# Kernel tuning notes

Hardware: AMD Instinct MI355X
Metric: run time of the kernel (lower is better)

Reference implementation:

```python
import jax, jax.numpy as jnp
import numpy as np

N_NODES = 100000
N_EDGES = 1600000
IN_FEATS = 64
HIDDEN = 128


def setup_inputs() -> dict:
    key = jax.random.key(0)
    k1, k2, k3, k4 = jax.random.split(key, 4)
    X = jax.random.normal(k1, (N_NODES, IN_FEATS), dtype=jnp.float32)
    edge_index = jax.random.randint(k2, (2, N_EDGES), 0, N_NODES, dtype=jnp.int64)
    W1 = jax.random.normal(k3, (IN_FEATS, HIDDEN), dtype=jnp.float32) * (1.0 / np.sqrt(IN_FEATS))
    b1 = jnp.zeros((HIDDEN,), dtype=jnp.float32)
    W2 = jax.random.normal(k4, (HIDDEN, 1), dtype=jnp.float32) * (1.0 / np.sqrt(HIDDEN))
    b2 = jnp.zeros((1,), dtype=jnp.float32)
    return {"X": X, "edge_index": edge_index, "W1": W1, "b1": b1, "W2": W2, "b2": b2}


def _gcn_conv(X, src, dst, norm, W, b, n_nodes):
    # GCNConv: out = D^{-1/2} (A + I) D^{-1/2} (X @ W) + b
    h = X @ W                       # [N, out_feats]
    msg = h[src] * norm[:, None]    # gather + per-edge scale
    out = jax.ops.segment_sum(msg, dst, num_segments=n_nodes)
    return out + b


def _norm_and_loops(edge_index, n_nodes):
    # add self loops and compute symmetric normalization coefficients
    loop = jnp.arange(n_nodes, dtype=edge_index.dtype)
    src = jnp.concatenate([edge_index[0], loop])
    dst = jnp.concatenate([edge_index[1], loop])
    deg = jax.ops.segment_sum(jnp.ones_like(dst, dtype=jnp.float32), dst,
                              num_segments=n_nodes)  # deg >= 1 (self loop)
    dinv = jax.lax.rsqrt(deg)
    norm = dinv[src] * dinv[dst]    # [E + N]
    return src, dst, norm


def reference(X, edge_index, W1, b1, W2, b2):
    n_nodes = X.shape[0]
    src, dst, norm = _norm_and_loops(edge_index, n_nodes)
    h = jax.nn.relu(_gcn_conv(X, src, dst, norm, W1, b1, n_nodes))
    # dropout omitted (stochastic; identity for deterministic reference)
    out = _gcn_conv(h, src, dst, norm, W2, b2, n_nodes)
    return out
```

## Files before the change

kernel.cpp:

```cpp
#include <hip/hip_runtime.h>
#include <hip/hip_fp16.h>


#define NNODES 100000
#define INF 64
#define HID 128
#define MAXBK 128
#define TILE_E 16384

using half8 = __attribute__((ext_vector_type(8))) _Float16;
using f32x4 = __attribute__((ext_vector_type(4))) float;

__global__ __launch_bounds__(1024) void k_thist(const int* __restrict__ dstA,
                                                int* __restrict__ tileCnt, int nE,
                                                const float* __restrict__ W1,
                                                _Float16* __restrict__ W1t, int nt) {
    __shared__ int h[MAXBK];
    int tid = threadIdx.x;
    int bx = blockIdx.x;
    if (bx == nt) {
        for (int i = tid; i < HID * INF; i += 1024) {
            int nCol = i >> 6;
            int k = i & 63;
            W1t[i] = (_Float16)W1[k * HID + nCol];
        }
        return;
    }
    if (tid < MAXBK) h[tid] = 0;
    __syncthreads();
    int base = bx * TILE_E;
#pragma unroll
    for (int k = 0; k < 16; ++k) {
        int e = base + k * 1024 + tid;
        if (e < nE) atomicAdd(&h[((unsigned)dstA[e]) >> 10], 1);
    }
    __syncthreads();
    if (tid < MAXBK) tileCnt[bx * MAXBK + tid] = h[tid];
}

__global__ __launch_bounds__(1024) void k_bscan(const int* __restrict__ tileCnt,
                                                int* __restrict__ tileBase,
                                                int* __restrict__ bBase,
                                                int* __restrict__ rowPtr,
                                                int n, int nbk, int nt) {
    __shared__ int part[8][MAXBK];
    __shared__ int colScan[MAXBK];
    int b = threadIdx.x & (MAXBK - 1);
    int tg = threadIdx.x >> 7;
    int cpg = (nt + 7) / 8;
    int tlo = tg * cpg, thi = min(tlo + cpg, nt);
    int sum = 0;
    for (int t = tlo; t < thi; ++t) sum += tileCnt[t * MAXBK + b];
    part[tg][b] = sum;
    __syncthreads();
    int coff = 0;
    for (int g = 0; g < tg; ++g) coff += part[g][b];
    int ctot = 0;
#pragma unroll
    for (int g = 0; g < 8; ++g) ctot += part[g][b];
    if (tg == 0) colScan[b] = ctot;
    __syncthreads();
    for (int off = 1; off < MAXBK; off <<= 1) {
        int u = (tg == 0 && b >= off) ? colScan[b - off] : 0;
        __syncthreads();
        if (tg == 0) colScan[b] += u;
        __syncthreads();
    }
    int colBase = colScan[b] - ctot;
    if (tg == 0 && b < nbk) bBase[b] = colBase;
    if (tg == 0 && b == nbk - 1) { bBase[nbk] = colScan[b]; rowPtr[n] = colScan[b]; }
    int run = colBase + coff;
    for (int t = tlo; t < thi; ++t) {
        tileBase[t * MAXBK + b] = run;
        run += tileCnt[t * MAXBK + b];
    }
}

__global__ __launch_bounds__(1024) void k_bin(const int* __restrict__ srcA,
                                              const int* __restrict__ dstA,
                                              const int* __restrict__ tileBase,
                                              unsigned* __restrict__ binned, int nE) {
    __shared__ int myb[MAXBK];
    __shared__ int cur[MAXBK];
    int tid = threadIdx.x;
    if (tid < MAXBK) {
        myb[tid] = tileBase[blockIdx.x * MAXBK + tid];
        cur[tid] = 0;
    }
    __syncthreads();
    int base = blockIdx.x * TILE_E;
#pragma unroll
    for (int k = 0; k < 16; ++k) {
        int e = base + k * 1024 + tid;
        if (e < nE) {
            int d = dstA[e];
            int s = srcA[e];
            int bk = ((unsigned)d) >> 10;
            int off = atomicAdd(&cur[bk], 1);
            binned[myb[bk] + off] = ((unsigned)(d & 1023) << 17) | (unsigned)s;
        }
    }
}

__global__ __launch_bounds__(1024) void k_csr(const unsigned* __restrict__ binned,
                                              const int* __restrict__ bBase,
                                              int* __restrict__ rowPtr,
                                              float* __restrict__ dinv,
                                              int* __restrict__ eSrc,
                                              const float4* __restrict__ X4,
                                              uint4* __restrict__ Xs4, int n) {
    __shared__ int hist[1024];
    __shared__ int curs[1024];
    int tid = threadIdx.x;
    int b = blockIdx.x;
    int lo = bBase[b], hi = bBase[b + 1];
    hist[tid] = 0;
    __syncthreads();
    for (int i = lo + tid; i < hi; i += 1024)
        atomicAdd(&hist[binned[i] >> 17], 1);
    __syncthreads();
    int own = hist[tid];
    for (int off = 1; off < 1024; off <<= 1) {
        int u = (tid >= off) ? hist[tid - off] : 0;
        __syncthreads();
        hist[tid] += u;
        __syncthreads();
    }
    int pos0 = lo + hist[tid] - own;
    curs[tid] = pos0;
    float dD = rsqrtf((float)(own + 1));
    hist[tid] = (int)__float_as_uint(dD);
    int node = (b << 10) + tid;
    if (node < n) {
        rowPtr[node] = pos0;
        dinv[node] = dD;
    }
    __syncthreads();
    for (int i = lo + tid; i < hi; i += 1024) {
        unsigned v = binned[i];
        int pos = atomicAdd(&curs[v >> 17], 1);
        eSrc[pos] = (int)(v & 0x1FFFFu);
    }
    __syncthreads();
    int nbase = b << 10;
#pragma unroll
    for (int k2 = 0; k2 < 8; ++k2) {
        int t2 = k2 * 1024 + tid;
        int nl = t2 >> 3;
        int r2 = t2 & 7;
        int node2 = nbase + nl;
        if (node2 < n) {
            float dD2 = __uint_as_float((unsigned)hist[nl]);
            float4 a = X4[(size_t)node2 * 16 + r2 * 2];
            float4 bb = X4[(size_t)node2 * 16 + r2 * 2 + 1];
            __half2 h0 = __float22half2_rn(make_float2(dD2 * a.x, dD2 * a.y));
            __half2 h1 = __float22half2_rn(make_float2(dD2 * a.z, dD2 * a.w));
            __half2 h2 = __float22half2_rn(make_float2(dD2 * bb.x, dD2 * bb.y));
            __half2 h3 = __float22half2_rn(make_float2(dD2 * bb.z, dD2 * bb.w));
            uint4 o;
            o.x = *(unsigned*)&h0; o.y = *(unsigned*)&h1;
            o.z = *(unsigned*)&h2; o.w = *(unsigned*)&h3;
            Xs4[(size_t)node2 * 8 + r2] = o;
        }
    }
}

__device__ inline void acc8_add(const uint4& v, float* acc) {
    const __half2* hp = (const __half2*)&v;
#pragma unroll
    for (int i = 0; i < 4; ++i) {
        float2 f = __half22float2(hp[i]);
        acc[2 * i]     += f.x;
        acc[2 * i + 1] += f.y;
    }
}

__global__ __launch_bounds__(256) void k_agg_mlp(const uint4* __restrict__ Xs4,
                                                 const int* __restrict__ rowPtr,
                                                 const int* __restrict__ eSrc,
                                                 const float* __restrict__ dinv,
                                                 const uint4* __restrict__ W1t4,
                                                 const float* __restrict__ b1,
                                                 const float* __restrict__ W2,
                                                 float* __restrict__ svs, int n) {
    __shared__ __align__(16) unsigned short W1s[HID * INF];
    __shared__ __align__(16) unsigned short aggS[32 * INF];
    __shared__ float b1s[HID];
    __shared__ float W2s[HID];
    int tid = threadIdx.x;

    for (int i = tid; i < HID * 8; i += 256) {
        int c = i >> 3, cb = i & 7;
        uint4 v = W1t4[i];
        int off = c * 128 + ((cb * 16) ^ ((c & 7) << 4));
        *(uint4*)((char*)W1s + off) = v;
    }
    if (tid < HID) {
        b1s[tid] = b1[tid];
        W2s[tid] = W2[tid];
    }

    int node0 = blockIdx.x * 32;
    int w = tid >> 3;
    int r = tid & 7;
    int node = node0 + w;
    if (node < n) {
        int beg = rowPtr[node];
        int end = rowPtr[node + 1];
        float dD = dinv[node];
        float acc[8];
        {
            uint4 v = Xs4[(size_t)node * 8 + r];
            const __half2* hp = (const __half2*)&v;
#pragma unroll
            for (int i = 0; i < 4; ++i) {
                float2 f = __half22float2(hp[i]);
                acc[2 * i] = f.x;
                acc[2 * i + 1] = f.y;
            }
        }
        int j = beg;
        int aEnd = min(end, (beg + 3) & ~3);
        for (; j < aEnd; ++j) {
            uint4 v = Xs4[(size_t)eSrc[j] * 8 + r];
            acc8_add(v, acc);
        }
        for (; j + 7 < end; j += 8) {
            int4 sa = *(const int4*)(eSrc + j);
            int4 sb = *(const int4*)(eSrc + j + 4);
            uint4 v0 = Xs4[(size_t)sa.x * 8 + r];
            uint4 v1 = Xs4[(size_t)sa.y * 8 + r];
            uint4 v2 = Xs4[(size_t)sa.z * 8 + r];
            uint4 v3 = Xs4[(size_t)sa.w * 8 + r];
            uint4 v4 = Xs4[(size_t)sb.x * 8 + r];
            uint4 v5 = Xs4[(size_t)sb.y * 8 + r];
            uint4 v6 = Xs4[(size_t)sb.z * 8 + r];
            uint4 v7 = Xs4[(size_t)sb.w * 8 + r];
            acc8_add(v0, acc); acc8_add(v1, acc); acc8_add(v2, acc); acc8_add(v3, acc);
            acc8_add(v4, acc); acc8_add(v5, acc); acc8_add(v6, acc); acc8_add(v7, acc);
        }
        if (j + 3 < end) {
            int4 s4 = *(const int4*)(eSrc + j);
            uint4 v0 = Xs4[(size_t)s4.x * 8 + r];
            uint4 v1 = Xs4[(size_t)s4.y * 8 + r];
            uint4 v2 = Xs4[(size_t)s4.z * 8 + r];
            uint4 v3 = Xs4[(size_t)s4.w * 8 + r];
            acc8_add(v0, acc); acc8_add(v1, acc); acc8_add(v2, acc); acc8_add(v3, acc);
            j += 4;
        }
        for (; j < end; ++j) {
            uint4 v = Xs4[(size_t)eSrc[j] * 8 + r];
            acc8_add(v, acc);
        }
        __half2 h0 = __float22half2_rn(make_float2(dD * acc[0], dD * acc[1]));
        __half2 h1 = __float22half2_rn(make_float2(dD * acc[2], dD * acc[3]));
        __half2 h2 = __float22half2_rn(make_float2(dD * acc[4], dD * acc[5]));
        __half2 h3 = __float22half2_rn(make_float2(dD * acc[6], dD * acc[7]));
        uint4 o;
        o.x = *(unsigned*)&h0; o.y = *(unsigned*)&h1;
        o.z = *(unsigned*)&h2; o.w = *(unsigned*)&h3;
        int off = w * 128 + ((r * 16) ^ ((w & 7) << 4));
        *(uint4*)((char*)aggS + off) = o;
    }
    __syncthreads();

    int wave = tid >> 6;
    if (wave < 2) {
        int l = tid & 63;
        int row16 = l & 15;
        int kg = l >> 4;
        int lrow = wave * 16 + row16;
        int swzA = (lrow & 7) << 4;
        half8 a0 = *(const half8*)((const char*)aggS + lrow * 128 + ((kg * 16) ^ swzA));
        half8 a1 = *(const half8*)((const char*)aggS + lrow * 128 + ((64 + kg * 16) ^ swzA));
        float p0 = 0.0f, p1 = 0.0f, p2 = 0.0f, p3 = 0.0f;
#pragma unroll
        for (int nt = 0; nt < 8; ++nt) {
            int c = nt * 16 + row16;
            int swzB = (c & 7) << 4;
            half8 bf0 = *(const half8*)((const char*)W1s + c * 128 + ((kg * 16) ^ swzB));
            half8 bf1 = *(const half8*)((const char*)W1s + c * 128 + ((64 + kg * 16) ^ swzB));
            f32x4 acc4 = {0.0f, 0.0f, 0.0f, 0.0f};
            acc4 = __builtin_amdgcn_mfma_f32_16x16x32_f16(a0, bf0, acc4, 0, 0, 0);
            acc4 = __builtin_amdgcn_mfma_f32_16x16x32_f16(a1, bf1, acc4, 0, 0, 0);
            float b1v = b1s[c];
            float w2v = W2s[c];
            float h;
            h = fmaxf(acc4[0] + b1v, 0.0f); p0 = fmaf(h, w2v, p0);
            h = fmaxf(acc4[1] + b1v, 0.0f); p1 = fmaf(h, w2v, p1);
            h = fmaxf(acc4[2] + b1v, 0.0f); p2 = fmaf(h, w2v, p2);
            h = fmaxf(acc4[3] + b1v, 0.0f); p3 = fmaf(h, w2v, p3);
        }
#pragma unroll
        for (int off = 1; off < 16; off <<= 1) {
            p0 += __shfl_xor(p0, off, 64);
            p1 += __shfl_xor(p1, off, 64);
            p2 += __shfl_xor(p2, off, 64);
            p3 += __shfl_xor(p3, off, 64);
        }
        if (row16 == 0) {
            int nd = node0 + wave * 16 + kg * 4;
            if (nd + 0 < n) svs[nd + 0] = dinv[nd + 0] * p0;
            if (nd + 1 < n) svs[nd + 1] = dinv[nd + 1] * p1;
            if (nd + 2 < n) svs[nd + 2] = dinv[nd + 2] * p2;
            if (nd + 3 < n) svs[nd + 3] = dinv[nd + 3] * p3;
        }
    }
}

__global__ __launch_bounds__(256) void k_out(const int* __restrict__ rowPtr,
                                             const int* __restrict__ eSrc,
                                             const float* __restrict__ dinv,
                                             const float* __restrict__ svs,
                                             const float* __restrict__ b2,
                                             float* __restrict__ out, int n) {
    int t = blockIdx.x * blockDim.x + threadIdx.x;
    int node = t >> 4;
    int r = t & 15;
    if (node >= n) return;
    int beg = rowPtr[node];
    int end = rowPtr[node + 1];
    float p = 0.0f;
    for (int j = beg + r; j < end; j += 16) p += svs[eSrc[j]];
    p += __shfl_xor(p, 1, 16);
    p += __shfl_xor(p, 2, 16);
    p += __shfl_xor(p, 4, 16);
    p += __shfl_xor(p, 8, 16);
    if (r == 0) {
        float dD = dinv[node];
        out[node] = fmaf(dD, p + svs[node], b2[0]);
    }
}

extern "C" void kernel_launch(void* const* d_in, const int* in_sizes, int n_in,
                              void* d_out, int out_size, void* d_ws, size_t ws_size,
                              hipStream_t stream) {
    const float* X  = (const float*)d_in[0];
    const int*   ei = (const int*)d_in[1];
    const float* W1 = (const float*)d_in[2];
    const float* b1 = (const float*)d_in[3];
    const float* W2 = (const float*)d_in[4];
    const float* b2 = (const float*)d_in[5];

    int N = in_sizes[0] / INF;
    int E = in_sizes[1] / 2;
    const int* srcA = ei;
    const int* dstA = ei + E;

    int nt  = (E + TILE_E - 1) / TILE_E;
    int nbk = (N + 1023) >> 10;

    uint4*    Xs4      = (uint4*)d_ws;
    unsigned* binned   = (unsigned*)(Xs4 + (size_t)N * 8);
    int*      eSrc     = (int*)(binned + E);
    _Float16* W1t      = (_Float16*)(eSrc + E);
    int*      tileCnt  = (int*)(W1t + HID * INF);
    int*      tileBase = tileCnt + nt * MAXBK;
    int*      bBase    = tileBase + nt * MAXBK;
    int*      rowPtr   = bBase + nbk + 1;
    float*    dinv     = (float*)(rowPtr + N + 1);
    float*    svs      = dinv + N;
    float*    out      = (float*)d_out;

    k_thist<<<nt + 1, 1024, 0, stream>>>(dstA, tileCnt, E, W1, W1t, nt);
    k_bscan<<<1, 1024, 0, stream>>>(tileCnt, tileBase, bBase, rowPtr, N, nbk, nt);
    k_bin<<<nt, 1024, 0, stream>>>(srcA, dstA, tileBase, binned, E);
    k_csr<<<nbk, 1024, 0, stream>>>(binned, bBase, rowPtr, dinv, eSrc,
                                    (const float4*)X, Xs4, N);
    k_agg_mlp<<<(N + 31) / 32, 256, 0, stream>>>(Xs4, rowPtr, eSrc, dinv,
                                                 (const uint4*)W1t, b1, W2, svs, N);
    k_out<<<(N * 16 + 255) / 256, 256, 0, stream>>>(rowPtr, eSrc, dinv, svs, b2, out, N);
}
```

Before: 113.1 us.

## Fuse edge histogram, scan and binning into one per-tile kernel

Replaces the three-kernel edge binning pipeline (tile histogram, single-block global scan, scatter) with one kernel. Each 8192-edge tile now scans its own bucket histogram locally and writes its binned edges into its own region, along with per-tile bucket offsets. The CSR kernel then gathers each bucket's segments from every tile and derives the bucket's global base by summing those offsets. Bucket size also shrinks from 1024 to 512 nodes, giving more CSR blocks. This removes two launches and the serial single-block scan, at the cost of many short, scattered segment reads per CSR block.

```diff
diff --git a/kernel.cpp b/kernel.cpp
--- a/kernel.cpp
+++ b/kernel.cpp
@@ -2,20 +2,23 @@
 #include <hip/hip_fp16.h>
 
 
-#define NNODES 100000
 #define INF 64
 #define HID 128
-#define MAXBK 128
-#define TILE_E 16384
+#define BKBITS 9
+#define BKSZ 512
+#define TILE_E 8192
+#define TOW 257
 
 using half8 = __attribute__((ext_vector_type(8))) _Float16;
 using f32x4 = __attribute__((ext_vector_type(4))) float;
 
-__global__ __launch_bounds__(1024) void k_thist(const int* __restrict__ dstA,
-                                                int* __restrict__ tileCnt, int nE,
-                                                const float* __restrict__ W1,
-                                                _Float16* __restrict__ W1t, int nt) {
-    __shared__ int h[MAXBK];
+__global__ __launch_bounds__(1024) void k_histbin(const int* __restrict__ srcA,
+                                                  const int* __restrict__ dstA,
+                                                  int* __restrict__ tileOff,
+                                                  unsigned* __restrict__ binned,
+                                                  int nE, int nt,
+                                                  const float* __restrict__ W1,
+                                                  _Float16* __restrict__ W1t) {
     int tid = threadIdx.x;
     int bx = blockIdx.x;
     if (bx == nt) {
@@ -26,131 +29,115 @@
         }
         return;
     }
-    if (tid < MAXBK) h[tid] = 0;
+    __shared__ int hist[256];
+    __shared__ int curs[256];
+    if (tid < 256) hist[tid] = 0;
     __syncthreads();
     int base = bx * TILE_E;
-#pragma unroll
-    for (int k = 0; k < 16; ++k) {
-        int e = base + k * 1024 + tid;
-        if (e < nE) atomicAdd(&h[((unsigned)dstA[e]) >> 10], 1);
-    }
-    __syncthreads();
-    if (tid < MAXBK) tileCnt[bx * MAXBK + tid] = h[tid];
-}
-
-__global__ __launch_bounds__(1024) void k_bscan(const int* __restrict__ tileCnt,
-                                                int* __restrict__ tileBase,
-                                                int* __restrict__ bBase,
-                                                int* __restrict__ rowPtr,
-                                                int n, int nbk, int nt) {
-    __shared__ int part[8][MAXBK];
-    __shared__ int colScan[MAXBK];
-    int b = threadIdx.x & (MAXBK - 1);
-    int tg = threadIdx.x >> 7;
-    int cpg = (nt + 7) / 8;
-    int tlo = tg * cpg, thi = min(tlo + cpg, nt);
-    int sum = 0;
-    for (int t = tlo; t < thi; ++t) sum += tileCnt[t * MAXBK + b];
-    part[tg][b] = sum;
-    __syncthreads();
-    int coff = 0;
-    for (int g = 0; g < tg; ++g) coff += part[g][b];
-    int ctot = 0;
-#pragma unroll
-    for (int g = 0; g < 8; ++g) ctot += part[g][b];
-    if (tg == 0) colScan[b] = ctot;
-    __syncthreads();
-    for (int off = 1; off < MAXBK; off <<= 1) {
-        int u = (tg == 0 && b >= off) ? colScan[b - off] : 0;
-        __syncthreads();
-        if (tg == 0) colScan[b] += u;
-        __syncthreads();
-    }
-    int colBase = colScan[b] - ctot;
-    if (tg == 0 && b < nbk) bBase[b] = colBase;
-    if (tg == 0 && b == nbk - 1) { bBase[nbk] = colScan[b]; rowPtr[n] = colScan[b]; }
-    int run = colBase + coff;
-    for (int t = tlo; t < thi; ++t) {
-        tileBase[t * MAXBK + b] = run;
-        run += tileCnt[t * MAXBK + b];
-    }
-}
-
-__global__ __launch_bounds__(1024) void k_bin(const int* __restrict__ srcA,
-                                              const int* __restrict__ dstA,
-                                              const int* __restrict__ tileBase,
-                                              unsigned* __restrict__ binned, int nE) {
-    __shared__ int myb[MAXBK];
-    __shared__ int cur[MAXBK];
-    int tid = threadIdx.x;
-    if (tid < MAXBK) {
-        myb[tid] = tileBase[blockIdx.x * MAXBK + tid];
-        cur[tid] = 0;
-    }
-    __syncthreads();
-    int base = blockIdx.x * TILE_E;
-#pragma unroll
-    for (int k = 0; k < 16; ++k) {
+    int d[8], s[8];
+#pragma unroll
+    for (int k = 0; k < 8; ++k) {
         int e = base + k * 1024 + tid;
         if (e < nE) {
-            int d = dstA[e];
-            int s = srcA[e];
-            int bk = ((unsigned)d) >> 10;
-            int off = atomicAdd(&cur[bk], 1);
-            binned[myb[bk] + off] = ((unsigned)(d & 1023) << 17) | (unsigned)s;
+            d[k] = dstA[e];
+            s[k] = srcA[e];
+            atomicAdd(&hist[((unsigned)d[k]) >> BKBITS], 1);
+        } else {
+            d[k] = -1;
+        }
+    }
+    __syncthreads();
+    int own = (tid < 256) ? hist[tid] : 0;
+    for (int off = 1; off < 256; off <<= 1) {
+        int u = (tid < 256 && tid >= off) ? hist[tid - off] : 0;
+        __syncthreads();
+        if (tid < 256) hist[tid] += u;
+        __syncthreads();
+    }
+    if (tid < 256) {
+        int ex = hist[tid] - own;
+        curs[tid] = ex;
+        tileOff[bx * TOW + tid] = ex;
+        if (tid == 255) tileOff[bx * TOW + 256] = hist[255];
+    }
+    __syncthreads();
+#pragma unroll
+    for (int k = 0; k < 8; ++k) {
+        if (d[k] >= 0) {
+            int bk = ((unsigned)d[k]) >> BKBITS;
+            int off = atomicAdd(&curs[bk], 1);
+            binned[base + off] = ((unsigned)(d[k] & (BKSZ - 1)) << 17) | (unsigned)s[k];
         }
     }
 }
 
 __global__ __launch_bounds__(1024) void k_csr(const unsigned* __restrict__ binned,
-                                              const int* __restrict__ bBase,
+                                              const int* __restrict__ tileOff,
                                               int* __restrict__ rowPtr,
                                               float* __restrict__ dinv,
                                               int* __restrict__ eSrc,
                                               const float4* __restrict__ X4,
-                                              uint4* __restrict__ Xs4, int n) {
-    __shared__ int hist[1024];
-    __shared__ int curs[1024];
+                                              uint4* __restrict__ Xs4,
+                                              int n, int nt, int nbk) {
+    __shared__ int segS[256], segL[256];
+    __shared__ int hist[512];
+    __shared__ int curs[512];
+    __shared__ float ddv[512];
+    __shared__ int bBaseS;
     int tid = threadIdx.x;
     int b = blockIdx.x;
-    int lo = bBase[b], hi = bBase[b + 1];
-    hist[tid] = 0;
-    __syncthreads();
-    for (int i = lo + tid; i < hi; i += 1024)
-        atomicAdd(&hist[binned[i] >> 17], 1);
-    __syncthreads();
-    int own = hist[tid];
-    for (int off = 1; off < 1024; off <<= 1) {
-        int u = (tid >= off) ? hist[tid - off] : 0;
+    if (tid == 0) bBaseS = 0;
+    if (tid < 512) hist[tid] = 0;
+    __syncthreads();
+    if (tid < nt) {
+        int o0 = tileOff[tid * TOW + b];
+        int o1 = tileOff[tid * TOW + b + 1];
+        segS[tid] = tid * TILE_E + o0;
+        segL[tid] = o1 - o0;
+        atomicAdd(&bBaseS, o0);
+    }
+    __syncthreads();
+    int w = tid >> 6, lane = tid & 63;
+    for (int t = w; t < nt; t += 16)
+        for (int l = lane; l < segL[t]; l += 64)
+            atomicAdd(&hist[binned[segS[t] + l] >> 17], 1);
+    __syncthreads();
+    int own = (tid < 512) ? hist[tid] : 0;
+    for (int off = 1; off < 512; off <<= 1) {
+        int u = (tid < 512 && tid >= off) ? hist[tid - off] : 0;
         __syncthreads();
-        hist[tid] += u;
+        if (tid < 512) hist[tid] += u;
         __syncthreads();
     }
-    int pos0 = lo + hist[tid] - own;
-    curs[tid] = pos0;
-    float dD = rsqrtf((float)(own + 1));
-    hist[tid] = (int)__float_as_uint(dD);
-    int node = (b << 10) + tid;
-    if (node < n) {
-        rowPtr[node] = pos0;
-        dinv[node] = dD;
-    }
-    __syncthreads();
-    for (int i = lo + tid; i < hi; i += 1024) {
-        unsigned v = binned[i];
-        int pos = atomicAdd(&curs[v >> 17], 1);
-        eSrc[pos] = (int)(v & 0x1FFFFu);
-    }
-    __syncthreads();
-    int nbase = b << 10;
-#pragma unroll
-    for (int k2 = 0; k2 < 8; ++k2) {
+    int bBase = bBaseS;
+    if (tid < 512) {
+        int pos0 = bBase + hist[tid] - own;
+        curs[tid] = pos0;
+        float dD = rsqrtf((float)(own + 1));
+        ddv[tid] = dD;
+        int node = (b << BKBITS) + tid;
+        if (node < n) {
+            rowPtr[node] = pos0;
+            dinv[node] = dD;
+        }
+        if (b == nbk - 1 && tid == 511) rowPtr[n] = bBase + hist[511];
+    }
+    __syncthreads();
+    for (int t = w; t < nt; t += 16)
+        for (int l = lane; l < segL[t]; l += 64) {
+            unsigned v = binned[segS[t] + l];
+            int pos = atomicAdd(&curs[v >> 17], 1);
+            eSrc[pos] = (int)(v & 0x1FFFFu);
+        }
+    int nbase = b << BKBITS;
+#pragma unroll
+    for (int k2 = 0; k2 < 4; ++k2) {
         int t2 = k2 * 1024 + tid;
         int nl = t2 >> 3;
         int r2 = t2 & 7;
         int node2 = nbase + nl;
         if (node2 < n) {
-            float dD2 = __uint_as_float((unsigned)hist[nl]);
+            float dD2 = ddv[nl];
             float4 a = X4[(size_t)node2 * 16 + r2 * 2];
             float4 bb = X4[(size_t)node2 * 16 + r2 * 2 + 1];
             __half2 h0 = __float22half2_rn(make_float2(dD2 * a.x, dD2 * a.y));
@@ -348,25 +335,21 @@
     const int* dstA = ei + E;
 
     int nt  = (E + TILE_E - 1) / TILE_E;
-    int nbk = (N + 1023) >> 10;
+    int nbk = (N + BKSZ - 1) >> BKBITS;
 
     uint4*    Xs4      = (uint4*)d_ws;
     unsigned* binned   = (unsigned*)(Xs4 + (size_t)N * 8);
-    int*      eSrc     = (int*)(binned + E);
+    int*      eSrc     = (int*)(binned + (size_t)nt * TILE_E);
     _Float16* W1t      = (_Float16*)(eSrc + E);
-    int*      tileCnt  = (int*)(W1t + HID * INF);
-    int*      tileBase = tileCnt + nt * MAXBK;
-    int*      bBase    = tileBase + nt * MAXBK;
-    int*      rowPtr   = bBase + nbk + 1;
+    int*      tileOff  = (int*)(W1t + HID * INF);
+    int*      rowPtr   = tileOff + nt * TOW;
     float*    dinv     = (float*)(rowPtr + N + 1);
     float*    svs      = dinv + N;
     float*    out      = (float*)d_out;
 
-    k_thist<<<nt + 1, 1024, 0, stream>>>(dstA, tileCnt, E, W1, W1t, nt);
-    k_bscan<<<1, 1024, 0, stream>>>(tileCnt, tileBase, bBase, rowPtr, N, nbk, nt);
-    k_bin<<<nt, 1024, 0, stream>>>(srcA, dstA, tileBase, binned, E);
-    k_csr<<<nbk, 1024, 0, stream>>>(binned, bBase, rowPtr, dinv, eSrc,
-                                    (const float4*)X, Xs4, N);
+    k_histbin<<<nt + 1, 1024, 0, stream>>>(srcA, dstA, tileOff, binned, E, nt, W1, W1t);
+    k_csr<<<nbk, 1024, 0, stream>>>(binned, tileOff, rowPtr, dinv, eSrc,
+                                    (const float4*)X, Xs4, N, nt, nbk);
     k_agg_mlp<<<(N + 31) / 32, 256, 0, stream>>>(Xs4, rowPtr, eSrc, dinv,
                                                  (const uint4*)W1t, b1, W2, svs, N);
     k_out<<<(N * 16 + 255) / 256, 256, 0, stream>>>(rowPtr, eSrc, dinv, svs, b2, out, N);
```

New measurement: 93.39 us (median of 2 runs). 1.21x faster.
